# Optimization experiments

Hardware: AMD Instinct MI355X
Metric: run time of the kernel (lower is better)

## Reference

```python
import jax, jax.numpy as jnp
import numpy as np

NUM_LAYERS = 3
INPUT_SIZE = 32
NUM_CAT = 64
EMB = 64
NQ = 1            # num_queries
B = 16
N = 2048
DIN = INPUT_SIZE + NUM_CAT + EMB  # 160, columns of W_e_proj


def setup_inputs() -> dict:
    key = jax.random.key(0)
    k1, k2, k3, k4 = jax.random.split(key, 4)
    return {
        "x": jax.random.normal(k1, (B, DIN, N), dtype=jnp.float32),
        "alpha": jax.random.normal(k2, (NUM_LAYERS, EMB), dtype=jnp.float32),
        "kernel_param": jnp.ones((1,), dtype=jnp.float32),
        "embedding_matrix": jax.random.normal(k3, (EMB, NUM_CAT), dtype=jnp.float32),
        "M": jax.random.normal(k4, (EMB, EMB), dtype=jnp.float32),
    }


def reference(x, alpha, kernel_param, embedding_matrix, M):
    # Input projection h = W_e_proj @ x. W_e_proj is block-structured:
    #   rows [0,is)        : identity on x[:is]
    #   rows [is, is+emb)  : embedding_matrix @ x[is:is+num_cat]
    #   rows [-emb:]       : identity on x[-emb:]
    h = jnp.concatenate([
        x[:, :INPUT_SIZE],
        jnp.einsum('ec,bcn->ben', embedding_matrix,
                   x[:, INPUT_SIZE:INPUT_SIZE + NUM_CAT]),
        x[:, -EMB:],
    ], axis=1)  # [B, INPUT_SIZE + 2*EMB, N]

    kp = kernel_param[0]
    for nl in range(NUM_LAYERS):
        kv = h[:, :, :-NQ]          # keys/values exclude the query tokens
        n_ctx = kv.shape[-1]
        # W_Q, W_K are identity on the first INPUT_SIZE rows, zero elsewhere
        xq = h[:, :INPUT_SIZE]      # [B, is, N]
        xk = kv[:, :INPUT_SIZE]     # [B, is, Nk]
        # linear kernel scores
        scores = kp * jnp.einsum('bim,bin->bmn', xq, xk)   # [B, N, Nk]
        # W_V is zero except diag(alpha[nl]) on the middle EMB block
        v_mid = alpha[nl][:, None] * kv[:, INPUT_SIZE:INPUT_SIZE + EMB]  # [B, EMB, Nk]
        attn_mid = jnp.einsum('bin,bmn->bim', v_mid, scores) / n_ctx     # [B, EMB, N]
        # Output projection P^T: middle rows get M @ attn_mid,
        # bottom EMB rows get attn_mid (identity), first rows zero.
        upd = jnp.concatenate([
            jnp.zeros((h.shape[0], INPUT_SIZE, h.shape[2]), h.dtype),
            jnp.einsum('ji,bim->bjm', M, attn_mid),
            attn_mid,
        ], axis=1)
        h = h + upd

    f = h[:, -EMB:, :]                                    # [B, EMB, N]
    logits = jnp.einsum('bdn,dc->bnc', f, embedding_matrix)  # [B, N, C]
    predictions = jax.nn.softmax(logits, axis=-1)
    return logits, predictions
```

## Files before the change

### kernel.cpp

```cpp
#include <hip/hip_runtime.h>

#define BB 16
#define NN 2048
#define DIN 160
#define IS 32
#define NCAT 64
#define EMBD 64
#define NCTX 2047
#define SS 66
#define NTILE 32
#define GRID1 (BB * NTILE)
#define NPART NTILE
#define USTRIDE (NPART * 1024)

__global__ __launch_bounds__(256) void k_gram(
    const float* __restrict__ x,
    float* __restrict__ Pg, float* __restrict__ Pk)
{
    __shared__ float xs[96 * SS];
    __shared__ float cbuf[3 * 64 * 52];
    const int t = threadIdx.x;
    const int blk = blockIdx.x;
    const int b = blk >> 5;
    const int tile = blk & 31;
    const int n0 = tile << 6;
    const float* xb = x + (size_t)b * DIN * NN;

    for (int idx = t; idx < 96 * 32; idx += 256) {
        const int r = idx >> 5;
        const int mc = (idx & 31) << 1;
        float2 v = *(const float2*)&xb[r * NN + n0 + mc];
        if (n0 + mc + 1 == NCTX) v.y = 0.f;
        *(float2*)&xs[r * SS + mc] = v;
    }
    __syncthreads();

    const int mg = t >> 6;
    const int lane = t & 63;
    const int i4 = lane >> 3;
    const int d4 = lane & 7;
    const int i0 = i4 << 2;
    const int d0 = d4 << 2;
    const int m0 = mg << 4;

    float g[4][4], kk[8][4];
#pragma unroll
    for (int ii = 0; ii < 4; ii++)
#pragma unroll
        for (int jj = 0; jj < 4; jj++) g[ii][jj] = 0.f;
#pragma unroll
    for (int ii = 0; ii < 8; ii++)
#pragma unroll
        for (int jj = 0; jj < 4; jj++) kk[ii][jj] = 0.f;

    for (int m = m0; m < m0 + 16; m += 2) {
        float2 q[4], a[4], c[8];
#pragma unroll
        for (int j = 0; j < 4; j++) q[j] = *(const float2*)&xs[(d0 + j) * SS + m];
#pragma unroll
        for (int j = 0; j < 4; j++) a[j] = *(const float2*)&xs[(i0 + j) * SS + m];
#pragma unroll
        for (int j = 0; j < 8; j++) c[j] = *(const float2*)&xs[(32 + i4 + 8 * j) * SS + m];
#pragma unroll
        for (int ii = 0; ii < 4; ii++)
#pragma unroll
            for (int jj = 0; jj < 4; jj++)
                g[ii][jj] += a[ii].x * q[jj].x + a[ii].y * q[jj].y;
#pragma unroll
        for (int ii = 0; ii < 8; ii++)
#pragma unroll
            for (int jj = 0; jj < 4; jj++)
                kk[ii][jj] += c[ii].x * q[jj].x + c[ii].y * q[jj].y;
    }

    if (mg > 0) {
        float* p = cbuf + ((mg - 1) * 64 + lane) * 52;
#pragma unroll
        for (int ii = 0; ii < 4; ii++) *(float4*)&p[ii * 4] = *(float4*)&g[ii][0];
#pragma unroll
        for (int ii = 0; ii < 8; ii++) *(float4*)&p[16 + ii * 4] = *(float4*)&kk[ii][0];
    }
    __syncthreads();
    if (mg == 0) {
#pragma unroll
        for (int w = 0; w < 3; w++) {
            const float* p = cbuf + (w * 64 + lane) * 52;
#pragma unroll
            for (int ii = 0; ii < 4; ii++) {
                float4 v = *(const float4*)&p[ii * 4];
                g[ii][0] += v.x; g[ii][1] += v.y; g[ii][2] += v.z; g[ii][3] += v.w;
            }
#pragma unroll
            for (int ii = 0; ii < 8; ii++) {
                float4 v = *(const float4*)&p[16 + ii * 4];
                kk[ii][0] += v.x; kk[ii][1] += v.y; kk[ii][2] += v.z; kk[ii][3] += v.w;
            }
        }
        float* pg = Pg + (size_t)blk * 1024;
#pragma unroll
        for (int ii = 0; ii < 4; ii++)
            *(float4*)&pg[(i0 + ii) * 32 + d0] = *(float4*)&g[ii][0];
        float* pk = Pk + (size_t)blk * 2048;
#pragma unroll
        for (int ii = 0; ii < 8; ii++)
            *(float4*)&pk[(i4 + 8 * ii) * 32 + d0] = *(float4*)&kk[ii][0];
    }
}

__global__ __launch_bounds__(256) void k_chain(
    float* PgU, const float* __restrict__ Pk,
    const float* __restrict__ alpha, const float* __restrict__ kp,
    const float* __restrict__ emb, const float* __restrict__ Mm)
{
    __shared__ float G_s[32][36];
    __shared__ float K_s[64][36];
    __shared__ float C_s[64][36];
    __shared__ float W_s[64][36];
    __shared__ float T_s[64][36];
    const int t = threadIdx.x;
    const int b = blockIdx.x;

    {
        const int row = t >> 3, col = (t & 7) << 2;
        float4 s = {0, 0, 0, 0};
        const float* base = PgU + (size_t)b * USTRIDE + row * 32 + col;
#pragma unroll 8
        for (int p = 0; p < NPART; p++) {
            float4 v = *(const float4*)(base + (size_t)p * 1024);
            s.x += v.x; s.y += v.y; s.z += v.z; s.w += v.w;
        }
        *(float4*)&G_s[row][col] = s;
    }
    {
        const int row0 = t >> 2, col = (t & 3) << 3;
        const float* base = Pk + (size_t)b * NPART * 2048 + row0 * 32 + col;
        float4 s0 = {0, 0, 0, 0}, s1 = {0, 0, 0, 0};
#pragma unroll 8
        for (int p = 0; p < NPART; p++) {
            float4 v0 = *(const float4*)(base + (size_t)p * 2048);
            float4 v1 = *(const float4*)(base + (size_t)p * 2048 + 4);
            s0.x += v0.x; s0.y += v0.y; s0.z += v0.z; s0.w += v0.w;
            s1.x += v1.x; s1.y += v1.y; s1.z += v1.z; s1.w += v1.w;
        }
        *(float4*)&K_s[row0][col] = s0;
        *(float4*)&K_s[row0][col + 4] = s1;
    }
    __syncthreads();

    const int r  = t >> 2;
    const int dd = (t & 3) << 3;
    {
        const float* er = emb + r * EMBD;
        float acc[8];
#pragma unroll
        for (int j = 0; j < 8; j++) acc[j] = 0.f;
        for (int c = 0; c < 64; c++) {
            const float e = er[c];
#pragma unroll
            for (int j = 0; j < 8; j++) acc[j] += e * K_s[c][dd + j];
        }
#pragma unroll
        for (int j = 0; j < 8; j++) C_s[r][dd + j] = acc[j];
    }
    __syncthreads();

    const float scale = kp[0] * (1.f / (float)NCTX);
    for (int l = 0; l < 3; l++) {
        const float f = scale * alpha[l * EMBD + r];
#pragma unroll
        for (int j = 0; j < 8; j++) {
            const float w = f * C_s[r][dd + j];
            if (l == 0) W_s[r][dd + j] = w; else W_s[r][dd + j] += w;
        }
        if (l < 2) {
            float tacc[8];
#pragma unroll
            for (int j = 0; j < 8; j++) tacc[j] = 0.f;
            for (int d = 0; d < 32; d++) {
                const float cv = C_s[r][d];
#pragma unroll
                for (int j = 0; j < 8; j++) tacc[j] += cv * G_s[d][dd + j];
            }
#pragma unroll
            for (int j = 0; j < 8; j++) T_s[r][dd + j] = f * tacc[j];
            __syncthreads();
            const float* Mr = Mm + r * EMBD;
            float uacc[8];
#pragma unroll
            for (int j = 0; j < 8; j++) uacc[j] = 0.f;
            for (int jj = 0; jj < 64; jj++) {
                const float mv = Mr[jj];
#pragma unroll
                for (int j = 0; j < 8; j++) uacc[j] += mv * T_s[jj][dd + j];
            }
#pragma unroll
            for (int j = 0; j < 8; j++) C_s[r][dd + j] += uacc[j];
            __syncthreads();
        }
    }
    __syncthreads();

    {
        float acc[8];
#pragma unroll
        for (int j = 0; j < 8; j++) acc[j] = 0.f;
        for (int e = 0; e < 64; e++) {
            const float ev = emb[e * EMBD + r];
#pragma unroll
            for (int j = 0; j < 8; j++) acc[j] += ev * W_s[e][dd + j];
        }
        float* ub = PgU + (size_t)b * USTRIDE + r * 32 + dd;
        float4 v0 = {acc[0], acc[1], acc[2], acc[3]};
        float4 v1 = {acc[4], acc[5], acc[6], acc[7]};
        *(float4*)&ub[0] = v0;
        *(float4*)&ub[4] = v1;
    }
}

__global__ __launch_bounds__(256) void k_out(
    const float* __restrict__ x, const float* __restrict__ Ug,
    const float* __restrict__ emb, float* __restrict__ out)
{
    __shared__ float U_s[64][32];
    __shared__ float xt_s[96 * SS];
    __shared__ float lg_s[64 * 65];
    const int t = threadIdx.x;
    const int blk = blockIdx.x;
    const int b = blk >> 5;
    const int tile = blk & 31;
    const int n0 = tile << 6;
    const float* xb = x + (size_t)b * DIN * NN;

    {
        const float* ub = Ug + (size_t)b * USTRIDE + t * 8;
        float4 v0 = *(const float4*)&ub[0];
        float4 v1 = *(const float4*)&ub[4];
        float* d = &U_s[0][0] + t * 8;
        *(float4*)&d[0] = v0;
        *(float4*)&d[4] = v1;
    }
    for (int idx = t; idx < 96 * 32; idx += 256) {
        const int r = idx >> 5;
        const int mc = (idx & 31) << 1;
        const int gr = (r < IS) ? r : (r + NCAT);
        float2 v = *(const float2*)&xb[gr * NN + n0 + mc];
        *(float2*)&xt_s[r * SS + mc] = v;
    }
    __syncthreads();

    const int nl = t & 63;
    const int h = t >> 6;
    const int c0 = h << 4;
    const int n = n0 + nl;

    float xq[IS];
#pragma unroll
    for (int d = 0; d < IS; d++) xq[d] = xt_s[d * SS + nl];

    float lg[16];
#pragma unroll
    for (int cl = 0; cl < 16; cl++) {
        const float* Ur = &U_s[c0 + cl][0];
        float s = 0.f;
#pragma unroll
        for (int k = 0; k < 8; k++) {
            float4 u = *(const float4*)&Ur[4 * k];
            s += u.x * xq[4*k] + u.y * xq[4*k+1] + u.z * xq[4*k+2] + u.w * xq[4*k+3];
        }
        lg[cl] = s;
    }
#pragma unroll 8
    for (int e = 0; e < 64; e++) {
        const float tv = xt_s[(IS + e) * SS + nl];
        const float* er = emb + e * EMBD + c0;
#pragma unroll
        for (int cl = 0; cl < 16; cl++) lg[cl] += er[cl] * tv;
    }

    const size_t base = ((size_t)b * NN + n) * (size_t)NCAT;
    float* lo = out + base + c0;
#pragma unroll
    for (int k = 0; k < 4; k++) {
        float4 v = {lg[4*k], lg[4*k+1], lg[4*k+2], lg[4*k+3]};
        *(float4*)&lo[4*k] = v;
    }
    float* ls = &lg_s[nl * 65 + c0];
#pragma unroll
    for (int cl = 0; cl < 16; cl++) ls[cl] = lg[cl];
    __syncthreads();

    float mx = lg[0];
#pragma unroll
    for (int cl = 1; cl < 16; cl++) mx = fmaxf(mx, lg[cl]);
    float og[48];
#pragma unroll
    for (int g = 1; g < 4; g++) {
        const int oc = ((h + g) & 3) << 4;
        const float* os = &lg_s[nl * 65 + oc];
#pragma unroll
        for (int cl = 0; cl < 16; cl++) {
            const float v = os[cl];
            og[(g - 1) * 16 + cl] = v;
            mx = fmaxf(mx, v);
        }
    }

    float sum = 0.f;
#pragma unroll
    for (int cl = 0; cl < 16; cl++) { lg[cl] = __expf(lg[cl] - mx); sum += lg[cl]; }
#pragma unroll
    for (int j = 0; j < 48; j++) sum += __expf(og[j] - mx);

    const float inv = 1.f / sum;
    float* po = out + (size_t)BB * NN * NCAT + base + c0;
#pragma unroll
    for (int k = 0; k < 4; k++) {
        float4 v = {lg[4*k]*inv, lg[4*k+1]*inv, lg[4*k+2]*inv, lg[4*k+3]*inv};
        *(float4*)&po[4*k] = v;
    }
}

extern "C" void kernel_launch(void* const* d_in, const int* in_sizes, int n_in,
                              void* d_out, int out_size, void* d_ws, size_t ws_size,
                              hipStream_t stream) {
    const float* x     = (const float*)d_in[0];
    const float* alpha = (const float*)d_in[1];
    const float* kp    = (const float*)d_in[2];
    const float* emb   = (const float*)d_in[3];
    const float* Mmat  = (const float*)d_in[4];
    float* out = (float*)d_out;

    float* Pg = (float*)d_ws;
    float* Pk = Pg + (size_t)GRID1 * 1024;

    k_gram <<<GRID1, 256, 0, stream>>>(x, Pg, Pk);
    k_chain<<<BB,    256, 0, stream>>>(Pg, Pk, alpha, kp, emb, Mmat);
    k_out  <<<512,   256, 0, stream>>>(x, Pg, emb, out);
}
```

Before: 127.7 us.

## Halve token tile to 32 and double block count in gram and output kernels

Both the Gram-partial kernel and the output/softmax kernel now process 32 tokens per block instead of 64, doubling the grid to 1024 blocks. The Gram kernel also aliases its staging and reduction shared buffers, with an extra barrier, to cut LDS use and allow more resident blocks. The output kernel restructures its softmax so each thread scans the full 64-wide logit row from shared memory. The intent is better CU occupancy and latency hiding, at the cost of more partial sums (NPART 64) for the chain kernel to reduce and some redundant exp work in the softmax.

Result: no change. 128.0 us (+0.3%).

```diff
diff --git a/kernel.cpp b/kernel.cpp
--- a/kernel.cpp
+++ b/kernel.cpp
@@ -7,31 +7,33 @@
 #define NCAT 64
 #define EMBD 64
 #define NCTX 2047
-#define SS 66
-#define NTILE 32
-#define GRID1 (BB * NTILE)
-#define NPART NTILE
+#define NT1 64
+#define GRID1 (BB * NT1)
+#define SS1 34
+#define NPART NT1
 #define USTRIDE (NPART * 1024)
-
-__global__ __launch_bounds__(256) void k_gram(
+#define SS2 34
+
+__global__ __launch_bounds__(256, 4) void k_gram(
     const float* __restrict__ x,
     float* __restrict__ Pg, float* __restrict__ Pk)
 {
-    __shared__ float xs[96 * SS];
-    __shared__ float cbuf[3 * 64 * 52];
+    __shared__ float smem[3 * 64 * 52];
+    float* xs = smem;
+    float* cbuf = smem;
     const int t = threadIdx.x;
     const int blk = blockIdx.x;
-    const int b = blk >> 5;
-    const int tile = blk & 31;
-    const int n0 = tile << 6;
+    const int b = blk >> 6;
+    const int tile = blk & 63;
+    const int n0 = tile << 5;
     const float* xb = x + (size_t)b * DIN * NN;
 
-    for (int idx = t; idx < 96 * 32; idx += 256) {
-        const int r = idx >> 5;
-        const int mc = (idx & 31) << 1;
+    for (int idx = t; idx < 96 * 16; idx += 256) {
+        const int r = idx >> 4;
+        const int mc = (idx & 15) << 1;
         float2 v = *(const float2*)&xb[r * NN + n0 + mc];
         if (n0 + mc + 1 == NCTX) v.y = 0.f;
-        *(float2*)&xs[r * SS + mc] = v;
+        *(float2*)&xs[r * SS1 + mc] = v;
     }
     __syncthreads();
 
@@ -41,7 +43,7 @@
     const int d4 = lane & 7;
     const int i0 = i4 << 2;
     const int d0 = d4 << 2;
-    const int m0 = mg << 4;
+    const int m0 = mg << 3;
 
     float g[4][4], kk[8][4];
 #pragma unroll
@@ -53,14 +55,14 @@
 #pragma unroll
         for (int jj = 0; jj < 4; jj++) kk[ii][jj] = 0.f;
 
-    for (int m = m0; m < m0 + 16; m += 2) {
+    for (int m = m0; m < m0 + 8; m += 2) {
         float2 q[4], a[4], c[8];
 #pragma unroll
-        for (int j = 0; j < 4; j++) q[j] = *(const float2*)&xs[(d0 + j) * SS + m];
-#pragma unroll
-        for (int j = 0; j < 4; j++) a[j] = *(const float2*)&xs[(i0 + j) * SS + m];
-#pragma unroll
-        for (int j = 0; j < 8; j++) c[j] = *(const float2*)&xs[(32 + i4 + 8 * j) * SS + m];
+        for (int j = 0; j < 4; j++) q[j] = *(const float2*)&xs[(d0 + j) * SS1 + m];
+#pragma unroll
+        for (int j = 0; j < 4; j++) a[j] = *(const float2*)&xs[(i0 + j) * SS1 + m];
+#pragma unroll
+        for (int j = 0; j < 8; j++) c[j] = *(const float2*)&xs[(32 + i4 + 8 * j) * SS1 + m];
 #pragma unroll
         for (int ii = 0; ii < 4; ii++)
 #pragma unroll
@@ -72,6 +74,8 @@
             for (int jj = 0; jj < 4; jj++)
                 kk[ii][jj] += c[ii].x * q[jj].x + c[ii].y * q[jj].y;
     }
+
+    __syncthreads();
 
     if (mg > 0) {
         float* p = cbuf + ((mg - 1) * 64 + lane) * 52;
@@ -217,18 +221,18 @@
     }
 }
 
-__global__ __launch_bounds__(256) void k_out(
+__global__ __launch_bounds__(256, 4) void k_out(
     const float* __restrict__ x, const float* __restrict__ Ug,
     const float* __restrict__ emb, float* __restrict__ out)
 {
     __shared__ float U_s[64][32];
-    __shared__ float xt_s[96 * SS];
-    __shared__ float lg_s[64 * 65];
+    __shared__ float xt_s[96 * SS2];
+    __shared__ float lg_s[32 * 65];
     const int t = threadIdx.x;
     const int blk = blockIdx.x;
-    const int b = blk >> 5;
-    const int tile = blk & 31;
-    const int n0 = tile << 6;
+    const int b = blk >> 6;
+    const int tile = blk & 63;
+    const int n0 = tile << 5;
     const float* xb = x + (size_t)b * DIN * NN;
 
     {
@@ -239,27 +243,27 @@
         *(float4*)&d[0] = v0;
         *(float4*)&d[4] = v1;
     }
-    for (int idx = t; idx < 96 * 32; idx += 256) {
-        const int r = idx >> 5;
-        const int mc = (idx & 31) << 1;
+    for (int idx = t; idx < 96 * 16; idx += 256) {
+        const int r = idx >> 4;
+        const int mc = (idx & 15) << 1;
         const int gr = (r < IS) ? r : (r + NCAT);
         float2 v = *(const float2*)&xb[gr * NN + n0 + mc];
-        *(float2*)&xt_s[r * SS + mc] = v;
-    }
-    __syncthreads();
-
-    const int nl = t & 63;
-    const int h = t >> 6;
-    const int c0 = h << 4;
+        *(float2*)&xt_s[r * SS2 + mc] = v;
+    }
+    __syncthreads();
+
+    const int nl = t & 31;
+    const int h = t >> 5;
+    const int c0 = h << 3;
     const int n = n0 + nl;
 
     float xq[IS];
 #pragma unroll
-    for (int d = 0; d < IS; d++) xq[d] = xt_s[d * SS + nl];
-
-    float lg[16];
-#pragma unroll
-    for (int cl = 0; cl < 16; cl++) {
+    for (int d = 0; d < IS; d++) xq[d] = xt_s[d * SS2 + nl];
+
+    float lg[8];
+#pragma unroll
+    for (int cl = 0; cl < 8; cl++) {
         const float* Ur = &U_s[c0 + cl][0];
         float s = 0.f;
 #pragma unroll
@@ -271,52 +275,48 @@
     }
 #pragma unroll 8
     for (int e = 0; e < 64; e++) {
-        const float tv = xt_s[(IS + e) * SS + nl];
+        const float tv = xt_s[(IS + e) * SS2 + nl];
         const float* er = emb + e * EMBD + c0;
-#pragma unroll
-        for (int cl = 0; cl < 16; cl++) lg[cl] += er[cl] * tv;
+        float4 e0 = *(const float4*)&er[0];
+        float4 e1 = *(const float4*)&er[4];
+        lg[0] += e0.x * tv; lg[1] += e0.y * tv; lg[2] += e0.z * tv; lg[3] += e0.w * tv;
+        lg[4] += e1.x * tv; lg[5] += e1.y * tv; lg[6] += e1.z * tv; lg[7] += e1.w * tv;
     }
 
     const size_t base = ((size_t)b * NN + n) * (size_t)NCAT;
     float* lo = out + base + c0;
-#pragma unroll
-    for (int k = 0; k < 4; k++) {
-        float4 v = {lg[4*k], lg[4*k+1], lg[4*k+2], lg[4*k+3]};
-        *(float4*)&lo[4*k] = v;
+    {
+        float4 v0 = {lg[0], lg[1], lg[2], lg[3]};
+        float4 v1 = {lg[4], lg[5], lg[6], lg[7]};
+        *(float4*)&lo[0] = v0;
+        *(float4*)&lo[4] = v1;
     }
     float* ls = &lg_s[nl * 65 + c0];
 #pragma unroll
-    for (int cl = 0; cl < 16; cl++) ls[cl] = lg[cl];
-    __syncthreads();
-
-    float mx = lg[0];
-#pragma unroll
-    for (int cl = 1; cl < 16; cl++) mx = fmaxf(mx, lg[cl]);
-    float og[48];
-#pragma unroll
-    for (int g = 1; g < 4; g++) {
-        const int oc = ((h + g) & 3) << 4;
-        const float* os = &lg_s[nl * 65 + oc];
-#pragma unroll
-        for (int cl = 0; cl < 16; cl++) {
-            const float v = os[cl];
-            og[(g - 1) * 16 + cl] = v;
-            mx = fmaxf(mx, v);
-        }
-    }
-
+    for (int cl = 0; cl < 8; cl++) ls[cl] = lg[cl];
+    __syncthreads();
+
+    const float* row = &lg_s[nl * 65];
+    float mx = row[0];
+#pragma unroll
+    for (int c = 1; c < 64; c++) mx = fmaxf(mx, row[c]);
+
+    float p[8];
     float sum = 0.f;
 #pragma unroll
-    for (int cl = 0; cl < 16; cl++) { lg[cl] = __expf(lg[cl] - mx); sum += lg[cl]; }
-#pragma unroll
-    for (int j = 0; j < 48; j++) sum += __expf(og[j] - mx);
+    for (int c = 0; c < 64; c++) {
+        const float e = __expf(row[c] - mx);
+        sum += e;
+        if ((c >> 3) == h) p[c & 7] = e;
+    }
 
     const float inv = 1.f / sum;
     float* po = out + (size_t)BB * NN * NCAT + base + c0;
-#pragma unroll
-    for (int k = 0; k < 4; k++) {
-        float4 v = {lg[4*k]*inv, lg[4*k+1]*inv, lg[4*k+2]*inv, lg[4*k+3]*inv};
-        *(float4*)&po[4*k] = v;
+    {
+        float4 v0 = {p[0]*inv, p[1]*inv, p[2]*inv, p[3]*inv};
+        float4 v1 = {p[4]*inv, p[5]*inv, p[6]*inv, p[7]*inv};
+        *(float4*)&po[0] = v0;
+        *(float4*)&po[4] = v1;
     }
 }
 
@@ -335,5 +335,5 @@
 
     k_gram <<<GRID1, 256, 0, stream>>>(x, Pg, Pk);
     k_chain<<<BB,    256, 0, stream>>>(Pg, Pk, alpha, kp, emb, Mmat);
-    k_out  <<<512,   256, 0, stream>>>(x, Pg, emb, out);
+    k_out  <<<BB*64, 256, 0, stream>>>(x, Pg, emb, out);
 }
```
